# Kernel optimization log

Hardware: AMD Instinct MI355X
Metric: run time of the kernel (lower is better)

## Reference

```python
import jax, jax.numpy as jnp
import numpy as np

GRID_SIZE = 5
SPLINE_ORDER = 3
NUM_BASIS = GRID_SIZE + SPLINE_ORDER  # 8
GRID = jnp.linspace(-1.0, 1.0, GRID_SIZE + 2 * SPLINE_ORDER + 1)  # [12]
EPS = 1e-6


def bspline_basis(x):
    """Iterative Cox-de Boor. x: [...]; returns [..., NUM_BASIS]."""
    xe = x[..., None]
    # order-0 indicator basis: [..., G-1]
    B = ((xe >= GRID[:-1]) & (xe < GRID[1:])).astype(x.dtype)
    for k in range(1, SPLINE_ORDER + 1):
        nb = B.shape[-1] - 1
        g_i = GRID[:nb]
        g_i1 = GRID[1:1 + nb]
        g_ik = GRID[k:k + nb]
        g_ik1 = GRID[k + 1:k + 1 + nb]
        dl = g_ik - g_i
        dr = g_ik1 - g_i1
        left = jnp.where(dl > EPS, (xe - g_i) / jnp.where(dl > EPS, dl, 1.0), 0.0) * B[..., :nb]
        right = jnp.where(dr > EPS, (g_ik1 - xe) / jnp.where(dr > EPS, dr, 1.0), 0.0) * B[..., 1:nb + 1]
        B = left + right
    return B[..., :NUM_BASIS]


def setup_inputs() -> dict:
    key = jax.random.key(0)
    k1, k2 = jax.random.split(key)
    x = jax.random.normal(k1, (8192, 512), dtype=jnp.float32)
    spline_coeffs = jax.random.normal(k2, (512, 512, NUM_BASIS), dtype=jnp.float32) * 0.1
    return {"x": x, "spline_coeffs": spline_coeffs}


def reference(x, spline_coeffs):
    xn = jnp.tanh(x)                       # [B, in]
    basis = bspline_basis(xn)              # [B, in, K]
    # output[b, o] = sum_{i,k} coeffs[o, i, k] * basis[b, i, k]
    return jnp.einsum('bik,oik->bo', basis, spline_coeffs)
```

## Files before the change

### kernel.cpp

```cpp
#include <hip/hip_runtime.h>
#include <hip/hip_bf16.h>
#include <stdint.h>


#define M_TOTAL 8192
#define N_DIM   512
#define K_DIM   4096
#define BM 128
#define BN 128
#define BK 64
#define NT_HALF 32
#define GRP_LDS 65536
#define BUF_HALF 32768

typedef __attribute__((ext_vector_type(8))) short short8;
typedef __attribute__((ext_vector_type(4))) float f32x4;

typedef const __attribute__((address_space(1))) uint32_t ga_u32;
typedef __attribute__((address_space(3))) uint32_t ls_u32;

__device__ __forceinline__ void gload_lds16(const void* g, void* l) {
  __builtin_amdgcn_global_load_lds((ga_u32*)(uintptr_t)g,
                                   (ls_u32*)(uint32_t)(uintptr_t)l, 16, 0, 0);
}

__device__ __forceinline__ uint32_t f2bf(float f) {
  uint32_t u = __builtin_bit_cast(uint32_t, f);
  return (u + 0x7FFFu + ((u >> 16) & 1u)) >> 16;
}

__device__ __forceinline__ void basis_slots(float xv, uint32_t o[4]) {
  xv = fminf(15.f, fmaxf(-15.f, xv));
  float e  = __expf(2.0f * xv);
  float t  = (e - 1.0f) * __builtin_amdgcn_rcpf(e + 1.0f);
  float uf = (t + 1.0f) * 5.5f;
  int   c  = (int)uf;  c = c > 10 ? 10 : c;
  float u  = uf - (float)c;
  float u2 = u * u, u3 = u2 * u, om = 1.0f - u;
  float w0 = om * om * om * (1.0f / 6.0f);
  float w1 = (3.0f * u3 - 6.0f * u2 + 4.0f) * (1.0f / 6.0f);
  float w2 = (-3.0f * u3 + 3.0f * u2 + 3.0f * u + 1.0f) * (1.0f / 6.0f);
  float w3 = u3 * (1.0f / 6.0f);
  uint32_t p01 = f2bf(w0) | (f2bf(w1) << 16);
  uint32_t p23 = f2bf(w2) | (f2bf(w3) << 16);
  uint64_t W = (uint64_t)p01 | ((uint64_t)p23 << 32);
  int d = c - 3;
  uint64_t lo = (d < 0) ? (W >> ((-d) * 16))
              : ((d < 4) ? (W << (d * 16)) : 0ull);
  uint64_t hi = (d <= 0) ? 0ull
              : ((d < 4) ? (W >> ((4 - d) * 16)) : (W << ((d - 4) * 16)));
  o[0] = (uint32_t)lo; o[1] = (uint32_t)(lo >> 32);
  o[2] = (uint32_t)hi; o[3] = (uint32_t)(hi >> 32);
}

__global__ __launch_bounds__(256) void basis_kernel(const float* __restrict__ x,
                                                    __hip_bfloat16* __restrict__ A,
                                                    int total) {
  int idx = blockIdx.x * 256 + threadIdx.x;
  if (idx >= total) return;
  uint32_t o[4];
  basis_slots(x[idx], o);
  reinterpret_cast<int4*>(A)[idx] = make_int4(o[0], o[1], o[2], o[3]);
}

__global__ __launch_bounds__(256) void cvt_kernel(const float* __restrict__ c,
                                                  __hip_bfloat16* __restrict__ Bt,
                                                  int total8) {
  int idx = blockIdx.x * 256 + threadIdx.x;
  if (idx >= total8) return;
  const float4* cp = reinterpret_cast<const float4*>(c) + (size_t)idx * 2;
  float4 a = cp[0], b = cp[1];
  union { unsigned short us[8]; int4 v; } pk;
  pk.us[0] = (unsigned short)f2bf(a.x); pk.us[1] = (unsigned short)f2bf(a.y);
  pk.us[2] = (unsigned short)f2bf(a.z); pk.us[3] = (unsigned short)f2bf(a.w);
  pk.us[4] = (unsigned short)f2bf(b.x); pk.us[5] = (unsigned short)f2bf(b.y);
  pk.us[6] = (unsigned short)f2bf(b.z); pk.us[7] = (unsigned short)f2bf(b.w);
  reinterpret_cast<int4*>(Bt)[idx] = pk.v;
}

__global__ __launch_bounds__(512) void gemm_kernel(
    const __hip_bfloat16* __restrict__ A,
    const __hip_bfloat16* __restrict__ Bt,
    float* __restrict__ C) {
  __shared__ char lds[2 * GRP_LDS];

  const int tid   = threadIdx.x;
  const int wid   = tid >> 6;
  const int lane  = tid & 63;
  const int quad  = lane >> 4;
  const int l16   = lane & 15;
  const int kgrp  = wid >> 2;
  const int w2    = wid & 3;
  const int waveM = w2 >> 1, waveN = w2 & 1;
  const int tg    = tid & 255;

  const int b  = blockIdx.x;
  const int q  = b >> 3;
  const int mt = (b & 7) * 8 + (q >> 2);
  const int nt = q & 3;
  const int m0 = mt * BM;
  const int n0 = nt * BN;

  char* grp = lds + kgrp * GRP_LDS;

  uint32_t aGlob[4], bGlob[4], sOff[4];
#pragma unroll
  for (int t = 0; t < 4; ++t) {
    int s = t * 256 + tg, row = s >> 3, p = s & 7, cc = p ^ (row & 7);
    sOff[t]  = (uint32_t)s * 16u;
    aGlob[t] = (uint32_t)(m0 + row) * K_DIM + (uint32_t)cc * 8u
             + (uint32_t)kgrp * 2048u;
    bGlob[t] = (uint32_t)(n0 + row) * K_DIM + (uint32_t)cc * 8u
             + (uint32_t)kgrp * 2048u;
  }

  uint32_t aOff[2][4], bOff[2][4];
#pragma unroll
  for (int kk = 0; kk < 2; ++kk) {
    int c = kk * 4 + quad;
#pragma unroll
    for (int mi = 0; mi < 4; ++mi) {
      int row = waveM * 64 + mi * 16 + l16;
      aOff[kk][mi] = (uint32_t)(row * 8 + (c ^ (row & 7))) * 16u;
    }
#pragma unroll
    for (int ni = 0; ni < 4; ++ni) {
      int row = waveN * 64 + ni * 16 + l16;
      bOff[kk][ni] = 16384u + (uint32_t)(row * 8 + (c ^ (row & 7))) * 16u;
    }
  }

  f32x4 acc[4][4];
#pragma unroll
  for (int mi = 0; mi < 4; ++mi)
#pragma unroll
    for (int ni = 0; ni < 4; ++ni)
      acc[mi][ni] = (f32x4){0.f, 0.f, 0.f, 0.f};

#pragma unroll
  for (int t = 0; t < 4; ++t) {
    gload_lds16(A + aGlob[t], grp + sOff[t]);
    gload_lds16(Bt + bGlob[t], grp + 16384 + sOff[t]);
  }

  for (int it = 0; it < NT_HALF; ++it) {
    const int cur = it & 1;
    char* bufc = grp + cur * BUF_HALF;
    __syncthreads();
    if (it + 1 < NT_HALF) {
      char* bufn = grp + (1 - cur) * BUF_HALF;
      uint32_t kt = (uint32_t)(it + 1) * BK;
#pragma unroll
      for (int t = 0; t < 4; ++t) {
        gload_lds16(A + aGlob[t] + kt, bufn + sOff[t]);
        gload_lds16(Bt + bGlob[t] + kt, bufn + 16384 + sOff[t]);
      }
    }
#pragma unroll
    for (int kk = 0; kk < 2; ++kk) {
      short8 af[4], bf[4];
#pragma unroll
      for (int mi = 0; mi < 4; ++mi)
        af[mi] = *reinterpret_cast<const short8*>(bufc + aOff[kk][mi]);
#pragma unroll
      for (int ni = 0; ni < 4; ++ni)
        bf[ni] = *reinterpret_cast<const short8*>(bufc + bOff[kk][ni]);
#pragma unroll
      for (int mi = 0; mi < 4; ++mi)
#pragma unroll
        for (int ni = 0; ni < 4; ++ni)
          acc[mi][ni] = __builtin_amdgcn_mfma_f32_16x16x32_bf16(
              af[mi], bf[ni], acc[mi][ni], 0, 0, 0);
    }
  }

  __syncthreads();
  if (kgrp == 1) {
#pragma unroll
    for (int mi = 0; mi < 4; ++mi)
#pragma unroll
      for (int ni = 0; ni < 4; ++ni) {
        int f = mi * 4 + ni;
        *reinterpret_cast<f32x4*>(lds + w2 * 16384 + f * 1024 + lane * 16) =
            acc[mi][ni];
      }
  }
  __syncthreads();
  if (kgrp == 0) {
#pragma unroll
    for (int mi = 0; mi < 4; ++mi) {
#pragma unroll
      for (int ni = 0; ni < 4; ++ni) {
        int f = mi * 4 + ni;
        f32x4 other = *reinterpret_cast<f32x4*>(
            lds + w2 * 16384 + f * 1024 + lane * 16);
        f32x4 s = acc[mi][ni] + other;
        int col = n0 + waveN * 64 + ni * 16 + l16;
#pragma unroll
        for (int r = 0; r < 4; ++r) {
          int row = m0 + waveM * 64 + mi * 16 + quad * 4 + r;
          C[(size_t)row * N_DIM + col] = s[r];
        }
      }
    }
  }
}

extern "C" void kernel_launch(void* const* d_in, const int* in_sizes, int n_in,
                              void* d_out, int out_size, void* d_ws, size_t ws_size,
                              hipStream_t stream) {
  const float* x    = (const float*)d_in[0];
  const float* coef = (const float*)d_in[1];
  float* out = (float*)d_out;

  __hip_bfloat16* Bt = (__hip_bfloat16*)d_ws;
  __hip_bfloat16* A  = (__hip_bfloat16*)((char*)d_ws + (size_t)4 * 1024 * 1024);

  const int total8 = N_DIM * K_DIM / 8;
  cvt_kernel<<<(total8 + 255) / 256, 256, 0, stream>>>(coef, Bt, total8);

  const int total = M_TOTAL * 512;
  basis_kernel<<<total / 256, 256, 0, stream>>>(x, A, total);

  gemm_kernel<<<(M_TOTAL / BM) * (N_DIM / BN), 512, 0, stream>>>(A, Bt, out);
}
```

Measured before the change: 118.2 us.

## Deepen GEMM K-pipeline to four LDS stages with explicit vmcnt waits

Replaces the double-buffered BK=64 main loop with a four-slot ring of BK=32 stages that keeps three loads in flight. Each iteration waits on vmcnt counts and a raw s_barrier instead of __syncthreads, and a new LDS swizzle packs two rows per 128-byte line. The aim is to hide global-to-LDS latency better. In exchange there are twice as many barriers per K, and fewer MFMAs sit between each pair of barriers.

Measured after the change: 125.7 us. 6.4% more time.

```diff
diff --git a/kernel.cpp b/kernel.cpp
--- a/kernel.cpp
+++ b/kernel.cpp
@@ -8,10 +8,11 @@
 #define K_DIM   4096
 #define BM 128
 #define BN 128
-#define BK 64
-#define NT_HALF 32
+#define BK 32
+#define NT_HALF 64
+#define PF 3
+#define BUF_SZ 16384
 #define GRP_LDS 65536
-#define BUF_HALF 32768
 
 typedef __attribute__((ext_vector_type(8))) short short8;
 typedef __attribute__((ext_vector_type(4))) float f32x4;
@@ -103,31 +104,35 @@
 
   char* grp = lds + kgrp * GRP_LDS;
 
-  uint32_t aGlob[4], bGlob[4], sOff[4];
-#pragma unroll
-  for (int t = 0; t < 4; ++t) {
-    int s = t * 256 + tg, row = s >> 3, p = s & 7, cc = p ^ (row & 7);
+  uint32_t aGlob[2], bGlob[2], sOff[2];
+#pragma unroll
+  for (int t = 0; t < 2; ++t) {
+    int s = t * 256 + tg;
+    int L = s >> 3, sl = s & 7;
+    int u = sl ^ (L & 7);
+    int r = L * 2 + (u >> 2);
+    int c = u & 3;
     sOff[t]  = (uint32_t)s * 16u;
-    aGlob[t] = (uint32_t)(m0 + row) * K_DIM + (uint32_t)cc * 8u
+    aGlob[t] = (uint32_t)(m0 + r) * K_DIM + (uint32_t)c * 8u
              + (uint32_t)kgrp * 2048u;
-    bGlob[t] = (uint32_t)(n0 + row) * K_DIM + (uint32_t)cc * 8u
+    bGlob[t] = (uint32_t)(n0 + r) * K_DIM + (uint32_t)c * 8u
              + (uint32_t)kgrp * 2048u;
   }
 
-  uint32_t aOff[2][4], bOff[2][4];
-#pragma unroll
-  for (int kk = 0; kk < 2; ++kk) {
-    int c = kk * 4 + quad;
-#pragma unroll
-    for (int mi = 0; mi < 4; ++mi) {
-      int row = waveM * 64 + mi * 16 + l16;
-      aOff[kk][mi] = (uint32_t)(row * 8 + (c ^ (row & 7))) * 16u;
-    }
-#pragma unroll
-    for (int ni = 0; ni < 4; ++ni) {
-      int row = waveN * 64 + ni * 16 + l16;
-      bOff[kk][ni] = 16384u + (uint32_t)(row * 8 + (c ^ (row & 7))) * 16u;
-    }
+  uint32_t aOff[4], bOff[4];
+#pragma unroll
+  for (int mi = 0; mi < 4; ++mi) {
+    int r = waveM * 64 + mi * 16 + l16;
+    int L = r >> 1;
+    int sl = (((r & 1) << 2) | quad) ^ (L & 7);
+    aOff[mi] = (uint32_t)(L * 8 + sl) * 16u;
+  }
+#pragma unroll
+  for (int ni = 0; ni < 4; ++ni) {
+    int r = waveN * 64 + ni * 16 + l16;
+    int L = r >> 1;
+    int sl = (((r & 1) << 2) | quad) ^ (L & 7);
+    bOff[ni] = 8192u + (uint32_t)(L * 8 + sl) * 16u;
   }
 
   f32x4 acc[4][4];
@@ -137,42 +142,50 @@
     for (int ni = 0; ni < 4; ++ni)
       acc[mi][ni] = (f32x4){0.f, 0.f, 0.f, 0.f};
 
-#pragma unroll
-  for (int t = 0; t < 4; ++t) {
-    gload_lds16(A + aGlob[t], grp + sOff[t]);
-    gload_lds16(Bt + bGlob[t], grp + 16384 + sOff[t]);
-  }
+#define STAGE(IT) do {                                                        \
+    char* bufn_ = grp + (((IT) & 3) * BUF_SZ);                                \
+    uint32_t kt_ = (uint32_t)(IT) * BK;                                       \
+    _Pragma("unroll")                                                         \
+    for (int t = 0; t < 2; ++t) {                                             \
+      gload_lds16(A + aGlob[t] + kt_, bufn_ + sOff[t]);                       \
+      gload_lds16(Bt + bGlob[t] + kt_, bufn_ + 8192 + sOff[t]);               \
+    }                                                                         \
+  } while (0)
+
+#pragma unroll
+  for (int p = 0; p < PF; ++p) STAGE(p);
 
   for (int it = 0; it < NT_HALF; ++it) {
-    const int cur = it & 1;
-    char* bufc = grp + cur * BUF_HALF;
-    __syncthreads();
-    if (it + 1 < NT_HALF) {
-      char* bufn = grp + (1 - cur) * BUF_HALF;
-      uint32_t kt = (uint32_t)(it + 1) * BK;
-#pragma unroll
-      for (int t = 0; t < 4; ++t) {
-        gload_lds16(A + aGlob[t] + kt, bufn + sOff[t]);
-        gload_lds16(Bt + bGlob[t] + kt, bufn + 16384 + sOff[t]);
-      }
+    char* bufc = grp + (it & 3) * BUF_SZ;
+    if (it + 3 < NT_HALF) {
+      STAGE(it + 3);
+      asm volatile("s_waitcnt vmcnt(12)" ::: "memory");
+    } else if (it + 2 < NT_HALF) {
+      asm volatile("s_waitcnt vmcnt(8)" ::: "memory");
+    } else if (it + 1 < NT_HALF) {
+      asm volatile("s_waitcnt vmcnt(4)" ::: "memory");
+    } else {
+      asm volatile("s_waitcnt vmcnt(0)" ::: "memory");
     }
-#pragma unroll
-    for (int kk = 0; kk < 2; ++kk) {
-      short8 af[4], bf[4];
-#pragma unroll
-      for (int mi = 0; mi < 4; ++mi)
-        af[mi] = *reinterpret_cast<const short8*>(bufc + aOff[kk][mi]);
+    __builtin_amdgcn_s_barrier();
+
+    short8 af[4], bf[4];
+#pragma unroll
+    for (int mi = 0; mi < 4; ++mi)
+      af[mi] = *reinterpret_cast<const short8*>(bufc + aOff[mi]);
+#pragma unroll
+    for (int ni = 0; ni < 4; ++ni)
+      bf[ni] = *reinterpret_cast<const short8*>(bufc + bOff[ni]);
+#pragma unroll
+    for (int mi = 0; mi < 4; ++mi)
 #pragma unroll
       for (int ni = 0; ni < 4; ++ni)
-        bf[ni] = *reinterpret_cast<const short8*>(bufc + bOff[kk][ni]);
-#pragma unroll
-      for (int mi = 0; mi < 4; ++mi)
-#pragma unroll
-        for (int ni = 0; ni < 4; ++ni)
-          acc[mi][ni] = __builtin_amdgcn_mfma_f32_16x16x32_bf16(
-              af[mi], bf[ni], acc[mi][ni], 0, 0, 0);
-    }
-  }
+        acc[mi][ni] = __builtin_amdgcn_mfma_f32_16x16x32_bf16(
+            af[mi], bf[ni], acc[mi][ni], 0, 0, 0);
+
+    __builtin_amdgcn_s_barrier();
+  }
+#undef STAGE
 
   __syncthreads();
   if (kgrp == 1) {
```

## Fuse B-spline basis expansion into GEMM A-tile producer

Applied to the files above, without the earlier changes.

Removes the separate basis kernel and its bf16 A matrix in workspace. The GEMM now reads raw x floats per tile, computes the cubic B-spline weights in-register, and writes the swizzled bf16 A tile into LDS, prefetching x one step ahead. This saves the 64MB A write and re-read through global memory, but recomputes the basis once per N-tile (4x redundant) and adds ALU work inside the main loop.

New measurement: 123.7 us. 1.05x slower.

```diff
diff --git a/kernel.cpp b/kernel.cpp
--- a/kernel.cpp
+++ b/kernel.cpp
@@ -53,16 +53,6 @@
   o[2] = (uint32_t)hi; o[3] = (uint32_t)(hi >> 32);
 }
 
-__global__ __launch_bounds__(256) void basis_kernel(const float* __restrict__ x,
-                                                    __hip_bfloat16* __restrict__ A,
-                                                    int total) {
-  int idx = blockIdx.x * 256 + threadIdx.x;
-  if (idx >= total) return;
-  uint32_t o[4];
-  basis_slots(x[idx], o);
-  reinterpret_cast<int4*>(A)[idx] = make_int4(o[0], o[1], o[2], o[3]);
-}
-
 __global__ __launch_bounds__(256) void cvt_kernel(const float* __restrict__ c,
                                                   __hip_bfloat16* __restrict__ Bt,
                                                   int total8) {
@@ -79,7 +69,7 @@
 }
 
 __global__ __launch_bounds__(512) void gemm_kernel(
-    const __hip_bfloat16* __restrict__ A,
+    const float* __restrict__ x,
     const __hip_bfloat16* __restrict__ Bt,
     float* __restrict__ C) {
   __shared__ char lds[2 * GRP_LDS];
@@ -103,13 +93,21 @@
 
   char* grp = lds + kgrp * GRP_LDS;
 
-  uint32_t aGlob[4], bGlob[4], sOff[4];
+  const int rA = tg >> 1;
+  const int c0 = (tg & 1) * 4;
+  const float* xp = x + (size_t)(m0 + rA) * N_DIM + (kgrp * 256 + c0);
+  uint32_t aW[4];
+#pragma unroll
+  for (int j = 0; j < 4; ++j) {
+    int p = (c0 + j) ^ (rA & 7);
+    aW[j] = (uint32_t)(rA * 128 + p * 16);
+  }
+
+  uint32_t bGlob[4], sOffB[4];
 #pragma unroll
   for (int t = 0; t < 4; ++t) {
     int s = t * 256 + tg, row = s >> 3, p = s & 7, cc = p ^ (row & 7);
-    sOff[t]  = (uint32_t)s * 16u;
-    aGlob[t] = (uint32_t)(m0 + row) * K_DIM + (uint32_t)cc * 8u
-             + (uint32_t)kgrp * 2048u;
+    sOffB[t] = (uint32_t)s * 16u;
     bGlob[t] = (uint32_t)(n0 + row) * K_DIM + (uint32_t)cc * 8u
              + (uint32_t)kgrp * 2048u;
   }
@@ -137,11 +135,20 @@
     for (int ni = 0; ni < 4; ++ni)
       acc[mi][ni] = (f32x4){0.f, 0.f, 0.f, 0.f};
 
-#pragma unroll
-  for (int t = 0; t < 4; ++t) {
-    gload_lds16(A + aGlob[t], grp + sOff[t]);
-    gload_lds16(Bt + bGlob[t], grp + 16384 + sOff[t]);
-  }
+  float4 xn = *reinterpret_cast<const float4*>(xp);
+  {
+    char* buf0 = grp;
+#pragma unroll
+    for (int j = 0; j < 4; ++j) {
+      uint32_t o[4];
+      basis_slots(j == 0 ? xn.x : j == 1 ? xn.y : j == 2 ? xn.z : xn.w, o);
+      *reinterpret_cast<int4*>(buf0 + aW[j]) = make_int4(o[0], o[1], o[2], o[3]);
+    }
+#pragma unroll
+    for (int t = 0; t < 4; ++t)
+      gload_lds16(Bt + bGlob[t], buf0 + 16384 + sOffB[t]);
+  }
+  xn = *reinterpret_cast<const float4*>(xp + 8);
 
   for (int it = 0; it < NT_HALF; ++it) {
     const int cur = it & 1;
@@ -149,12 +156,20 @@
     __syncthreads();
     if (it + 1 < NT_HALF) {
       char* bufn = grp + (1 - cur) * BUF_HALF;
+      int nx = it + 2 < NT_HALF ? it + 2 : NT_HALF - 1;
+      float4 xt = *reinterpret_cast<const float4*>(xp + (size_t)nx * 8);
+#pragma unroll
+      for (int j = 0; j < 4; ++j) {
+        uint32_t o[4];
+        basis_slots(j == 0 ? xn.x : j == 1 ? xn.y : j == 2 ? xn.z : xn.w, o);
+        *reinterpret_cast<int4*>(bufn + aW[j]) =
+            make_int4(o[0], o[1], o[2], o[3]);
+      }
       uint32_t kt = (uint32_t)(it + 1) * BK;
 #pragma unroll
-      for (int t = 0; t < 4; ++t) {
-        gload_lds16(A + aGlob[t] + kt, bufn + sOff[t]);
-        gload_lds16(Bt + bGlob[t] + kt, bufn + 16384 + sOff[t]);
-      }
+      for (int t = 0; t < 4; ++t)
+        gload_lds16(Bt + bGlob[t] + kt, bufn + 16384 + sOffB[t]);
+      xn = xt;
     }
 #pragma unroll
     for (int kk = 0; kk < 2; ++kk) {
@@ -214,13 +229,9 @@
   float* out = (float*)d_out;
 
   __hip_bfloat16* Bt = (__hip_bfloat16*)d_ws;
-  __hip_bfloat16* A  = (__hip_bfloat16*)((char*)d_ws + (size_t)4 * 1024 * 1024);
 
   const int total8 = N_DIM * K_DIM / 8;
   cvt_kernel<<<(total8 + 255) / 256, 256, 0, stream>>>(coef, Bt, total8);
 
-  const int total = M_TOTAL * 512;
-  basis_kernel<<<total / 256, 256, 0, stream>>>(x, A, total);
-
-  gemm_kernel<<<(M_TOTAL / BM) * (N_DIM / BN), 512, 0, stream>>>(A, Bt, out);
-}
+  gemm_kernel<<<(M_TOTAL / BM) * (N_DIM / BN), 512, 0, stream>>>(x, Bt, out);
+}
```

## Shrink GEMM N-tile to 64 and load B fragments directly into registers

Applied to the files above, without the earlier changes.

The GEMM tile drops from 128x128 to 128x64 and the block shrinks to 256 threads (4 waves: 2 M-waves by 2 K-split groups). Only A is staged through LDS. Each wave reads its B fragments straight from global memory into registers, software-prefetched one K-step ahead. This halves LDS use per block and doubles the block count to raise occupancy and cut LDS traffic. The cost is uncoalesced 16-byte global loads for B, repeated by every block sharing the N-tile and not shared between waves through LDS, plus extra register pressure.

After: 162.3 us. 1.37x slower.

```diff
diff --git a/kernel.cpp b/kernel.cpp
--- a/kernel.cpp
+++ b/kernel.cpp
@@ -7,11 +7,10 @@
 #define N_DIM   512
 #define K_DIM   4096
 #define BM 128
-#define BN 128
+#define BN 64
 #define BK 64
 #define NT_HALF 32
-#define GRP_LDS 65536
-#define BUF_HALF 32768
+#define GRP_LDS 32768
 
 typedef __attribute__((ext_vector_type(8))) short short8;
 typedef __attribute__((ext_vector_type(4))) float f32x4;
@@ -78,7 +77,7 @@
   reinterpret_cast<int4*>(Bt)[idx] = pk.v;
 }
 
-__global__ __launch_bounds__(512) void gemm_kernel(
+__global__ __launch_bounds__(256) void gemm_kernel(
     const __hip_bfloat16* __restrict__ A,
     const __hip_bfloat16* __restrict__ Bt,
     float* __restrict__ C) {
@@ -89,32 +88,29 @@
   const int lane  = tid & 63;
   const int quad  = lane >> 4;
   const int l16   = lane & 15;
-  const int kgrp  = wid >> 2;
-  const int w2    = wid & 3;
-  const int waveM = w2 >> 1, waveN = w2 & 1;
-  const int tg    = tid & 255;
+  const int kgrp  = wid >> 1;
+  const int waveM = wid & 1;
+  const int tgg   = tid & 127;
 
   const int b  = blockIdx.x;
-  const int q  = b >> 3;
-  const int mt = (b & 7) * 8 + (q >> 2);
-  const int nt = q & 3;
+  const int s  = b >> 3;
+  const int mt = (b & 7) * 8 + (s >> 3);
+  const int nt = s & 7;
   const int m0 = mt * BM;
   const int n0 = nt * BN;
 
   char* grp = lds + kgrp * GRP_LDS;
 
-  uint32_t aGlob[4], bGlob[4], sOff[4];
-#pragma unroll
-  for (int t = 0; t < 4; ++t) {
-    int s = t * 256 + tg, row = s >> 3, p = s & 7, cc = p ^ (row & 7);
-    sOff[t]  = (uint32_t)s * 16u;
+  uint32_t aGlob[8], sOff[8];
+#pragma unroll
+  for (int t = 0; t < 8; ++t) {
+    int s_ = t * 128 + tgg, row = s_ >> 3, p = s_ & 7, cc = p ^ (row & 7);
+    sOff[t]  = (uint32_t)s_ * 16u;
     aGlob[t] = (uint32_t)(m0 + row) * K_DIM + (uint32_t)cc * 8u
              + (uint32_t)kgrp * 2048u;
-    bGlob[t] = (uint32_t)(n0 + row) * K_DIM + (uint32_t)cc * 8u
-             + (uint32_t)kgrp * 2048u;
-  }
-
-  uint32_t aOff[2][4], bOff[2][4];
+  }
+
+  uint32_t aOff[2][4];
 #pragma unroll
   for (int kk = 0; kk < 2; ++kk) {
     int c = kk * 4 + quad;
@@ -123,12 +119,17 @@
       int row = waveM * 64 + mi * 16 + l16;
       aOff[kk][mi] = (uint32_t)(row * 8 + (c ^ (row & 7))) * 16u;
     }
+  }
+
+  uint32_t bIdx[2][4];
+#pragma unroll
+  for (int kk = 0; kk < 2; ++kk)
 #pragma unroll
     for (int ni = 0; ni < 4; ++ni) {
-      int row = waveN * 64 + ni * 16 + l16;
-      bOff[kk][ni] = 16384u + (uint32_t)(row * 8 + (c ^ (row & 7))) * 16u;
-    }
-  }
+      int r = n0 + ni * 16 + l16;
+      bIdx[kk][ni] = (uint32_t)r * K_DIM + (uint32_t)kgrp * 2048u
+                   + (uint32_t)(kk * 32 + quad * 8);
+    }
 
   f32x4 acc[4][4];
 #pragma unroll
@@ -137,40 +138,58 @@
     for (int ni = 0; ni < 4; ++ni)
       acc[mi][ni] = (f32x4){0.f, 0.f, 0.f, 0.f};
 
-#pragma unroll
-  for (int t = 0; t < 4; ++t) {
+  short8 bfA[4], bfB[4];
+#pragma unroll
+  for (int t = 0; t < 8; ++t)
     gload_lds16(A + aGlob[t], grp + sOff[t]);
-    gload_lds16(Bt + bGlob[t], grp + 16384 + sOff[t]);
+#pragma unroll
+  for (int ni = 0; ni < 4; ++ni) {
+    bfA[ni] = *reinterpret_cast<const short8*>(Bt + bIdx[0][ni]);
+    bfB[ni] = *reinterpret_cast<const short8*>(Bt + bIdx[1][ni]);
   }
 
   for (int it = 0; it < NT_HALF; ++it) {
-    const int cur = it & 1;
-    char* bufc = grp + cur * BUF_HALF;
+    char* bufc = grp + (it & 1) * 16384;
     __syncthreads();
     if (it + 1 < NT_HALF) {
-      char* bufn = grp + (1 - cur) * BUF_HALF;
+      char* bufn = grp + ((it + 1) & 1) * 16384;
       uint32_t kt = (uint32_t)(it + 1) * BK;
 #pragma unroll
-      for (int t = 0; t < 4; ++t) {
+      for (int t = 0; t < 8; ++t)
         gload_lds16(A + aGlob[t] + kt, bufn + sOff[t]);
-        gload_lds16(Bt + bGlob[t] + kt, bufn + 16384 + sOff[t]);
-      }
-    }
-#pragma unroll
-    for (int kk = 0; kk < 2; ++kk) {
-      short8 af[4], bf[4];
-#pragma unroll
-      for (int mi = 0; mi < 4; ++mi)
-        af[mi] = *reinterpret_cast<const short8*>(bufc + aOff[kk][mi]);
-#pragma unroll
-      for (int ni = 0; ni < 4; ++ni)
-        bf[ni] = *reinterpret_cast<const short8*>(bufc + bOff[kk][ni]);
-#pragma unroll
-      for (int mi = 0; mi < 4; ++mi)
-#pragma unroll
-        for (int ni = 0; ni < 4; ++ni)
-          acc[mi][ni] = __builtin_amdgcn_mfma_f32_16x16x32_bf16(
-              af[mi], bf[ni], acc[mi][ni], 0, 0, 0);
+    }
+
+    short8 af[4];
+#pragma unroll
+    for (int mi = 0; mi < 4; ++mi)
+      af[mi] = *reinterpret_cast<const short8*>(bufc + aOff[0][mi]);
+#pragma unroll
+    for (int mi = 0; mi < 4; ++mi)
+#pragma unroll
+      for (int ni = 0; ni < 4; ++ni)
+        acc[mi][ni] = __builtin_amdgcn_mfma_f32_16x16x32_bf16(
+            af[mi], bfA[ni], acc[mi][ni], 0, 0, 0);
+    if (it + 1 < NT_HALF) {
+      uint32_t kt = (uint32_t)(it + 1) * BK;
+#pragma unroll
+      for (int ni = 0; ni < 4; ++ni)
+        bfA[ni] = *reinterpret_cast<const short8*>(Bt + bIdx[0][ni] + kt);
+    }
+
+#pragma unroll
+    for (int mi = 0; mi < 4; ++mi)
+      af[mi] = *reinterpret_cast<const short8*>(bufc + aOff[1][mi]);
+#pragma unroll
+    for (int mi = 0; mi < 4; ++mi)
+#pragma unroll
+      for (int ni = 0; ni < 4; ++ni)
+        acc[mi][ni] = __builtin_amdgcn_mfma_f32_16x16x32_bf16(
+            af[mi], bfB[ni], acc[mi][ni], 0, 0, 0);
+    if (it + 1 < NT_HALF) {
+      uint32_t kt = (uint32_t)(it + 1) * BK;
+#pragma unroll
+      for (int ni = 0; ni < 4; ++ni)
+        bfB[ni] = *reinterpret_cast<const short8*>(Bt + bIdx[1][ni] + kt);
     }
   }
 
@@ -181,7 +200,7 @@
 #pragma unroll
       for (int ni = 0; ni < 4; ++ni) {
         int f = mi * 4 + ni;
-        *reinterpret_cast<f32x4*>(lds + w2 * 16384 + f * 1024 + lane * 16) =
+        *reinterpret_cast<f32x4*>(lds + waveM * 16384 + f * 1024 + lane * 16) =
             acc[mi][ni];
       }
   }
@@ -193,13 +212,13 @@
       for (int ni = 0; ni < 4; ++ni) {
         int f = mi * 4 + ni;
         f32x4 other = *reinterpret_cast<f32x4*>(
-            lds + w2 * 16384 + f * 1024 + lane * 16);
-        f32x4 s = acc[mi][ni] + other;
-        int col = n0 + waveN * 64 + ni * 16 + l16;
+            lds + waveM * 16384 + f * 1024 + lane * 16);
+        f32x4 s2 = acc[mi][ni] + other;
+        int col = n0 + ni * 16 + l16;
 #pragma unroll
         for (int r = 0; r < 4; ++r) {
           int row = m0 + waveM * 64 + mi * 16 + quad * 4 + r;
-          C[(size_t)row * N_DIM + col] = s[r];
+          C[(size_t)row * N_DIM + col] = s2[r];
         }
       }
     }
@@ -222,5 +241,5 @@
   const int total = M_TOTAL * 512;
   basis_kernel<<<total / 256, 256, 0, stream>>>(x, A, total);
 
-  gemm_kernel<<<(M_TOTAL / BM) * (N_DIM / BN), 512, 0, stream>>>(A, Bt, out);
-}
+  gemm_kernel<<<(M_TOTAL / BM) * (N_DIM / BN), 256, 0, stream>>>(A, Bt, out);
+}
```
